# Optimization experiments

Hardware: AMD Instinct MI355X
Metric: run time of the kernel (lower is better)

Reference implementation:

```python
import jax, jax.numpy as jnp
import numpy as np

N_NODES = 100000
N_EDGES = 1600000
C_IN = 64
C_OUT = 64
BN_EPS = 1e-5


def setup_inputs() -> dict:
    key = jax.random.key(0)
    k_x, k_e, k_w, k_b, k_g = jax.random.split(key, 5)
    x = jax.random.normal(k_x, (N_NODES, C_IN), dtype=jnp.float32)
    edge_index = jax.random.randint(k_e, (2, N_EDGES), 0, N_NODES, dtype=jnp.int64)
    # Linear(in_channels*2, out_channels)
    lim = 1.0 / np.sqrt(2 * C_IN)
    W = jax.random.uniform(k_w, (2 * C_IN, C_OUT), dtype=jnp.float32, minval=-lim, maxval=lim)
    b = jax.random.uniform(k_b, (C_OUT,), dtype=jnp.float32, minval=-lim, maxval=lim)
    # BatchNorm affine params
    gamma = jnp.ones((C_OUT,), dtype=jnp.float32)
    beta = jnp.zeros((C_OUT,), dtype=jnp.float32)
    return {"x": x, "edge_index": edge_index, "W": W, "b": b, "gamma": gamma, "beta": beta}


def reference(x, edge_index, W, b, gamma, beta):
    src = edge_index[0]  # j (source)
    dst = edge_index[1]  # i (target)
    x_i = x[dst]                      # [E, C_IN]
    x_j = x[src]                      # [E, C_IN]
    # EdgeConv message: mlp(concat(x_i, x_j - x_i))
    feat = jnp.concatenate([x_i, x_j - x_i], axis=-1)  # [E, 2*C_IN]
    msg = feat @ W + b                                  # [E, C_OUT]
    # max aggregation back to target nodes; empty nodes -> 0 (PyG convention)
    agg = jax.ops.segment_max(msg, dst, num_segments=N_NODES)
    agg = jnp.where(jnp.isneginf(agg), 0.0, agg)
    h = jax.nn.elu(agg)
    # BatchNorm1d over nodes (training-mode batch stats, biased variance)
    mean = jnp.mean(h, axis=0)
    var = jnp.var(h, axis=0)
    return gamma * (h - mean) / jnp.sqrt(var + BN_EPS) + beta
```

## Files before the change

### kernel.cpp

```cpp
#include <hip/hip_runtime.h>
#include <math.h>

#define N_NODES 100000
#define N_EDGES 1600000
#define C 64
#define BKT_SHIFT 6
#define BKT_NODES 64
#define NBKT 1563
#define BKT_CAP 2048
#define TILE 8192
#define NBINB 196
#define NGEMB 391
#define MAXW 65
#define NSTRIPE 32
#define XSTR 72
#define BN_EPS 1e-5f

typedef __attribute__((ext_vector_type(8))) short short8;
typedef __attribute__((ext_vector_type(4))) float f32x4;


__device__ __forceinline__ float eluf(float x) {
    return x > 0.f ? x : (expf(x) - 1.f);
}
__device__ __forceinline__ float key32_to_f(unsigned k32) {
    unsigned k16 = k32 >> 16;
    unsigned u16 = (k16 & 0x8000u) ? (k16 & 0x7FFFu) : (~k16 & 0xFFFFu);
    return __uint_as_float(u16 << 16);
}
__device__ __forceinline__ unsigned bf16rne(float f) {
    unsigned u = __float_as_uint(f);
    return (u + 0x7FFFu + ((u >> 16) & 1u)) >> 16;
}
__device__ __forceinline__ float bf16lo_f(unsigned w) { return __uint_as_float((w & 0xFFFFu) << 16); }
__device__ __forceinline__ float bf16hi_f(unsigned w) { return __uint_as_float(w & 0xFFFF0000u); }

__device__ __forceinline__ short8 pack8(float4 a, float4 b) {
    short8 r;
    r[0] = (short)bf16rne(a.x); r[1] = (short)bf16rne(a.y);
    r[2] = (short)bf16rne(a.z); r[3] = (short)bf16rne(a.w);
    r[4] = (short)bf16rne(b.x); r[5] = (short)bf16rne(b.y);
    r[6] = (short)bf16rne(b.z); r[7] = (short)bf16rne(b.w);
    return r;
}

__global__ __launch_bounds__(256) void k_init(unsigned* __restrict__ bcnt,
                                              float* __restrict__ stripes) {
    int t = blockIdx.x * blockDim.x + threadIdx.x;
    if (t < NBKT) bcnt[t] = 0u;
    if (t < NSTRIPE * 128) stripes[t] = 0.f;
}

__global__ __launch_bounds__(1024) void k_prep(const int* __restrict__ ei,
                                               const float* __restrict__ x,
                                               const float* __restrict__ W,
                                               const float* __restrict__ b,
                                               unsigned* __restrict__ bcnt,
                                               unsigned* __restrict__ binned,
                                               unsigned* __restrict__ Apb,
                                               unsigned* __restrict__ Bkey) {
    __shared__ __align__(16) unsigned char smem[18688];
    int t = threadIdx.x;

    if (blockIdx.x < NBINB) {
        unsigned* hcnt = (unsigned*)smem;
        unsigned* hbase = hcnt + NBKT;
        int e0 = blockIdx.x * TILE;
        int ecount = min(TILE, N_EDGES - e0);

        for (int i = t; i < NBKT; i += 1024) hcnt[i] = 0u;
        __syncthreads();
        for (int i = t; i < ecount; i += 1024) {
            int dst = ei[N_EDGES + e0 + i];
            if ((unsigned)dst < N_NODES) atomicAdd(&hcnt[dst >> BKT_SHIFT], 1u);
        }
        __syncthreads();
        for (int i = t; i < NBKT; i += 1024) {
            unsigned c = hcnt[i];
            hbase[i] = c ? atomicAdd(&bcnt[i], c) : 0u;
            hcnt[i] = 0u;
        }
        __syncthreads();
        for (int i = t; i < ecount; i += 1024) {
            int src = ei[e0 + i];
            int dst = ei[N_EDGES + e0 + i];
            if ((unsigned)src >= N_NODES || (unsigned)dst >= N_NODES) continue;
            int bk = dst >> BKT_SHIFT;
            unsigned pos = hbase[bk] + atomicAdd(&hcnt[bk], 1u);
            if (pos < BKT_CAP)
                binned[(size_t)bk * BKT_CAP + pos] =
                    ((unsigned)(dst & (BKT_NODES - 1)) << 17) | (unsigned)src;
        }
    } else {
        unsigned short* WaT = (unsigned short*)smem;
        unsigned short* WbT = WaT + 64 * XSTR;
        float* biasS = (float*)(WbT + 64 * XSTR);
        int gb = blockIdx.x - NBINB;
        int base = gb * 256;

        for (int p = t; p < 4096; p += 1024) {
            int k = p >> 6, c = p & 63;
            float w1 = W[p];
            float w2 = W[4096 + p];
            WaT[c * XSTR + k] = (unsigned short)bf16rne(w1 - w2);
            WbT[c * XSTR + k] = (unsigned short)bf16rne(w2);
        }
        if (t < 64) biasS[t] = b[t];
        __syncthreads();

        int w = t >> 6;
        int l = t & 63;
        int ln = l & 15;
        int hi = l >> 4;

        short8 wa[4][2], wb[4][2];
#pragma unroll
        for (int nt = 0; nt < 4; ++nt)
#pragma unroll
            for (int h = 0; h < 2; ++h) {
                wa[nt][h] = *(const short8*)&WaT[(nt * 16 + ln) * XSTR + h * 32 + hi * 8];
                wb[nt][h] = *(const short8*)&WbT[(nt * 16 + ln) * XSTR + h * 32 + hi * 8];
            }

        int arow = base + w * 16 + ln;
        short8 af[2];
        if (arow < N_NODES) {
            const float4* xr = (const float4*)(x + (size_t)arow * 64);
#pragma unroll
            for (int h = 0; h < 2; ++h)
                af[h] = pack8(xr[h * 8 + hi * 2], xr[h * 8 + hi * 2 + 1]);
        } else {
#pragma unroll
            for (int h = 0; h < 2; ++h)
                af[h] = (short8){0, 0, 0, 0, 0, 0, 0, 0};
        }

        f32x4 acca[4], accb[4];
#pragma unroll
        for (int nt = 0; nt < 4; ++nt) {
            acca[nt] = (f32x4){0.f, 0.f, 0.f, 0.f};
            accb[nt] = (f32x4){0.f, 0.f, 0.f, 0.f};
#pragma unroll
            for (int h = 0; h < 2; ++h) {
                acca[nt] = __builtin_amdgcn_mfma_f32_16x16x32_bf16(af[h], wa[nt][h], acca[nt], 0, 0, 0);
                accb[nt] = __builtin_amdgcn_mfma_f32_16x16x32_bf16(af[h], wb[nt][h], accb[nt], 0, 0, 0);
            }
        }
#pragma unroll
        for (int nt = 0; nt < 4; ++nt) {
            int col = nt * 16 + ln;
            float bias = biasS[col];
            int cp = nt * 8 + (ln >> 1);
#pragma unroll
            for (int r = 0; r < 4; ++r) {
                int node = base + w * 16 + hi * 4 + r;
                unsigned a16 = bf16rne(acca[nt][r] + bias);
                unsigned aO = (unsigned)__shfl_xor((int)a16, 1, 64);
                unsigned r16 = bf16rne(accb[nt][r]);
                unsigned key16 = (r16 & 0x8000u) ? (~r16 & 0xFFFFu) : (r16 | 0x8000u);
                unsigned kO = (unsigned)__shfl_xor((int)key16, 1, 64);
                if (((l & 1) == 0) && node < N_NODES) {
                    Apb[(size_t)node * 32 + cp] = a16 | (aO << 16);
                    Bkey[(size_t)node * 32 + cp] = key16 | (kO << 16);
                }
            }
        }
    }
}

__global__ __launch_bounds__(256) void k_fused(const unsigned* __restrict__ bcnt,
                                               const unsigned* __restrict__ binned,
                                               const unsigned* __restrict__ Bkey,
                                               const unsigned* __restrict__ Apb,
                                               unsigned* __restrict__ hpk,
                                               float* __restrict__ stripes) {
    __shared__ __align__(16) unsigned mx[BKT_NODES * MAXW];
    int q = blockIdx.x;
    int t = threadIdx.x;
    int n0 = q * BKT_NODES;
    int nspan = min(BKT_NODES, N_NODES - n0);

    for (int i = t; i < BKT_NODES * MAXW; i += 256) mx[i] = 0u;
    __syncthreads();

    unsigned cnt = min(bcnt[q], (unsigned)BKT_CAP);
    const unsigned* lst = binned + (size_t)q * BKT_CAP;
    int ls = t & 3;
    for (unsigned i = (unsigned)(t >> 2); i < cnt; i += 64) {
        unsigned p = lst[i];
        unsigned src = p & 0x1FFFFu;
        unsigned dl = p >> 17;
        const uint4* bk = (const uint4*)(Bkey + (size_t)src * 32);
        uint4 w0 = bk[ls];
        uint4 w1 = bk[4 + ls];
        unsigned* row = mx + dl * MAXW;
        int s0 = ls * 8;
        atomicMax(&row[s0 + 0], w0.x << 16);
        atomicMax(&row[s0 + 1], w0.x & 0xFFFF0000u);
        atomicMax(&row[s0 + 2], w0.y << 16);
        atomicMax(&row[s0 + 3], w0.y & 0xFFFF0000u);
        atomicMax(&row[s0 + 4], w0.z << 16);
        atomicMax(&row[s0 + 5], w0.z & 0xFFFF0000u);
        atomicMax(&row[s0 + 6], w0.w << 16);
        atomicMax(&row[s0 + 7], w0.w & 0xFFFF0000u);
        int s1 = 32 + ls * 8;
        atomicMax(&row[s1 + 0], w1.x << 16);
        atomicMax(&row[s1 + 1], w1.x & 0xFFFF0000u);
        atomicMax(&row[s1 + 2], w1.y << 16);
        atomicMax(&row[s1 + 3], w1.y & 0xFFFF0000u);
        atomicMax(&row[s1 + 4], w1.z << 16);
        atomicMax(&row[s1 + 5], w1.z & 0xFFFF0000u);
        atomicMax(&row[s1 + 6], w1.w << 16);
        atomicMax(&row[s1 + 7], w1.w & 0xFFFF0000u);
    }
    __syncthreads();

    int lane4 = t & 15;
    int g = t >> 4;
    float4 s = make_float4(0.f, 0.f, 0.f, 0.f);
    float4 sq = make_float4(0.f, 0.f, 0.f, 0.f);
    for (int nl = g; nl < nspan; nl += 16) {
        int n = n0 + nl;
        const unsigned* row = mx + nl * MAXW + lane4 * 4;
        unsigned k0 = row[0], k1 = row[1], k2 = row[2], k3 = row[3];
        uint2 ap = *reinterpret_cast<const uint2*>(Apb + (size_t)n * 32 + lane4 * 2);
        float h0 = (k0 == 0u) ? 0.f : eluf(bf16lo_f(ap.x) + key32_to_f(k0));
        float h1 = (k1 == 0u) ? 0.f : eluf(bf16hi_f(ap.x) + key32_to_f(k1));
        float h2 = (k2 == 0u) ? 0.f : eluf(bf16lo_f(ap.y) + key32_to_f(k2));
        float h3 = (k3 == 0u) ? 0.f : eluf(bf16hi_f(ap.y) + key32_to_f(k3));
        unsigned q0 = bf16rne(h0), q1 = bf16rne(h1), q2 = bf16rne(h2), q3 = bf16rne(h3);
        uint2 hp;
        hp.x = q0 | (q1 << 16);
        hp.y = q2 | (q3 << 16);
        *reinterpret_cast<uint2*>(hpk + (size_t)n * 32 + lane4 * 2) = hp;
        float f0 = __uint_as_float(q0 << 16), f1 = __uint_as_float(q1 << 16);
        float f2 = __uint_as_float(q2 << 16), f3 = __uint_as_float(q3 << 16);
        s.x += f0; s.y += f1; s.z += f2; s.w += f3;
        sq.x += f0 * f0; sq.y += f1 * f1; sq.z += f2 * f2; sq.w += f3 * f3;
    }
    __syncthreads();

    float4* lsum = (float4*)mx;
    float4* lqum = lsum + 256;
    lsum[t] = s;
    lqum[t] = sq;
    __syncthreads();
#pragma unroll
    for (int off = 8; off >= 1; off >>= 1) {
        if (g < off) {
            int o = t + off * 16;
            lsum[t].x += lsum[o].x; lsum[t].y += lsum[o].y; lsum[t].z += lsum[o].z; lsum[t].w += lsum[o].w;
            lqum[t].x += lqum[o].x; lqum[t].y += lqum[o].y; lqum[t].z += lqum[o].z; lqum[t].w += lqum[o].w;
        }
        __syncthreads();
    }
    if (g == 0) {
        float* sb = stripes + (q & (NSTRIPE - 1)) * 128;
        int c4 = lane4 * 4;
        atomicAdd(&sb[c4 + 0], lsum[t].x);
        atomicAdd(&sb[c4 + 1], lsum[t].y);
        atomicAdd(&sb[c4 + 2], lsum[t].z);
        atomicAdd(&sb[c4 + 3], lsum[t].w);
        atomicAdd(&sb[64 + c4 + 0], lqum[t].x);
        atomicAdd(&sb[64 + c4 + 1], lqum[t].y);
        atomicAdd(&sb[64 + c4 + 2], lqum[t].z);
        atomicAdd(&sb[64 + c4 + 3], lqum[t].w);
    }
}

__global__ __launch_bounds__(128) void k_reduce(const float* __restrict__ stripes,
                                                float* __restrict__ finals) {
    int t = threadIdx.x;
    float acc = 0.f;
#pragma unroll
    for (int s = 0; s < NSTRIPE; ++s) acc += stripes[s * 128 + t];
    finals[t] = acc;
}

__global__ __launch_bounds__(256) void k_bn(const uint2* __restrict__ hpk2,
                                            const float* __restrict__ finals,
                                            const float* __restrict__ gamma,
                                            const float* __restrict__ beta,
                                            float4* __restrict__ out4) {
    size_t i = (size_t)blockIdx.x * blockDim.x + threadIdx.x;
    size_t stride = (size_t)gridDim.x * blockDim.x;
    const float invN = 1.f / (float)N_NODES;
    size_t total4 = (size_t)N_NODES * C / 4;
    for (size_t p = i; p < total4; p += stride) {
        int c4 = (int)(p & 15) * 4;
        uint2 hp = hpk2[p];
        float hx = bf16lo_f(hp.x), hy = bf16hi_f(hp.x);
        float hz = bf16lo_f(hp.y), hw = bf16hi_f(hp.y);
        float4 o;
        float m, v, inv;
        m = finals[c4 + 0] * invN; v = finals[64 + c4 + 0] * invN - m * m; inv = rsqrtf(v + BN_EPS);
        o.x = gamma[c4 + 0] * (hx - m) * inv + beta[c4 + 0];
        m = finals[c4 + 1] * invN; v = finals[64 + c4 + 1] * invN - m * m; inv = rsqrtf(v + BN_EPS);
        o.y = gamma[c4 + 1] * (hy - m) * inv + beta[c4 + 1];
        m = finals[c4 + 2] * invN; v = finals[64 + c4 + 2] * invN - m * m; inv = rsqrtf(v + BN_EPS);
        o.z = gamma[c4 + 2] * (hz - m) * inv + beta[c4 + 2];
        m = finals[c4 + 3] * invN; v = finals[64 + c4 + 3] * invN - m * m; inv = rsqrtf(v + BN_EPS);
        o.w = gamma[c4 + 3] * (hw - m) * inv + beta[c4 + 3];
        out4[p] = o;
    }
}

extern "C" void kernel_launch(void* const* d_in, const int* in_sizes, int n_in,
                              void* d_out, int out_size, void* d_ws, size_t ws_size,
                              hipStream_t stream) {
    const float* x = (const float*)d_in[0];
    const int* ei = (const int*)d_in[1];
    const float* W = (const float*)d_in[2];
    const float* b = (const float*)d_in[3];
    const float* gamma = (const float*)d_in[4];
    const float* beta = (const float*)d_in[5];
    float* out = (float*)d_out;

    char* ws = (char*)d_ws;
    unsigned* Bkey = (unsigned*)ws;
    unsigned* binned = (unsigned*)(ws + (size_t)N_NODES * 32 * 4);
    unsigned* Apb = (unsigned*)((char*)binned + (size_t)NBKT * BKT_CAP * 4);
    unsigned* hpk = Apb + (size_t)N_NODES * 32;
    unsigned* bcnt = hpk + (size_t)N_NODES * 32;
    float* stripes = (float*)((char*)bcnt + ((NBKT * 4 + 255) & ~255));
    float* finals = stripes + NSTRIPE * 128;

    k_init<<<(NSTRIPE * 128 + NBKT + 255) / 256, 256, 0, stream>>>(bcnt, stripes);
    k_prep<<<NBINB + NGEMB, 1024, 0, stream>>>(ei, x, W, b, bcnt, binned, Apb, Bkey);
    k_fused<<<NBKT, 256, 0, stream>>>(bcnt, binned, Bkey, Apb, hpk, stripes);
    k_reduce<<<1, 128, 0, stream>>>(stripes, finals);
    k_bn<<<2048, 256, 0, stream>>>((const uint2*)hpk, finals, gamma, beta, (float4*)out);
}
```

Before: 86.11 us.

## Replace global-atomic bucket binning with per-tile prefix tables and XCD-aware block remap

A new histogram kernel computes, for each edge tile, a per-bucket exclusive prefix table. The binning pass then writes edges into tile-local contiguous ranges without global atomics or a fixed bucket capacity. The aggregation kernel rebuilds each bucket's edge list by prefix-summing the 196 tile ranges and binary-searching per edge. Blocks are also remapped so that consecutive buckets land on the same XCD. This removes global atomic contention and overflow truncation, at the cost of an extra pass over the edge indices, scans in shared memory, and scattered reads of the binned data.

New measurement: 84.99 us. Within noise of the previous version (-1.3%).

```diff
diff --git a/kernel.cpp b/kernel.cpp
--- a/kernel.cpp
+++ b/kernel.cpp
@@ -7,10 +7,10 @@
 #define BKT_SHIFT 6
 #define BKT_NODES 64
 #define NBKT 1563
-#define BKT_CAP 2048
 #define TILE 8192
 #define NBINB 196
 #define NGEMB 391
+#define PSTR 1564
 #define MAXW 65
 #define NSTRIPE 32
 #define XSTR 72
@@ -44,18 +44,51 @@
     return r;
 }
 
-__global__ __launch_bounds__(256) void k_init(unsigned* __restrict__ bcnt,
-                                              float* __restrict__ stripes) {
-    int t = blockIdx.x * blockDim.x + threadIdx.x;
-    if (t < NBKT) bcnt[t] = 0u;
-    if (t < NSTRIPE * 128) stripes[t] = 0.f;
+__global__ __launch_bounds__(1024) void k_hist(const int* __restrict__ ei,
+                                               unsigned* __restrict__ tab,
+                                               float* __restrict__ stripes) {
+    __shared__ unsigned hc[NBKT];
+    __shared__ unsigned ss[1024];
+    int t = threadIdx.x;
+    int tile = blockIdx.x;
+    int e0 = tile * TILE;
+    int ecount = min(TILE, N_EDGES - e0);
+
+    for (int i = t; i < NBKT; i += 1024) hc[i] = 0u;
+    if (blockIdx.x == 0) {
+        for (int i = t; i < NSTRIPE * 128; i += 1024) stripes[i] = 0.f;
+    }
+    __syncthreads();
+    for (int i = t; i < ecount; i += 1024) {
+        int src = ei[e0 + i];
+        int dst = ei[N_EDGES + e0 + i];
+        if ((unsigned)src < N_NODES && (unsigned)dst < N_NODES)
+            atomicAdd(&hc[dst >> BKT_SHIFT], 1u);
+    }
+    __syncthreads();
+    unsigned v0 = (2 * t < NBKT) ? hc[2 * t] : 0u;
+    unsigned v1 = (2 * t + 1 < NBKT) ? hc[2 * t + 1] : 0u;
+    unsigned s = v0 + v1;
+    ss[t] = s;
+    __syncthreads();
+    for (int off = 1; off < 1024; off <<= 1) {
+        unsigned v = (t >= off) ? ss[t - off] : 0u;
+        __syncthreads();
+        ss[t] += v;
+        __syncthreads();
+    }
+    unsigned excl = ss[t] - s;
+    unsigned* row = tab + (size_t)tile * PSTR;
+    if (2 * t < NBKT) row[2 * t] = excl;
+    if (2 * t + 1 < NBKT) row[2 * t + 1] = excl + v0;
+    if (t == 1023) row[NBKT] = ss[1023];
 }
 
 __global__ __launch_bounds__(1024) void k_prep(const int* __restrict__ ei,
                                                const float* __restrict__ x,
                                                const float* __restrict__ W,
                                                const float* __restrict__ b,
-                                               unsigned* __restrict__ bcnt,
+                                               const unsigned* __restrict__ tab,
                                                unsigned* __restrict__ binned,
                                                unsigned* __restrict__ Apb,
                                                unsigned* __restrict__ Bkey) {
@@ -63,33 +96,21 @@
     int t = threadIdx.x;
 
     if (blockIdx.x < NBINB) {
-        unsigned* hcnt = (unsigned*)smem;
-        unsigned* hbase = hcnt + NBKT;
-        int e0 = blockIdx.x * TILE;
+        unsigned* cur = (unsigned*)smem;
+        int tile = blockIdx.x;
+        int e0 = tile * TILE;
         int ecount = min(TILE, N_EDGES - e0);
-
-        for (int i = t; i < NBKT; i += 1024) hcnt[i] = 0u;
-        __syncthreads();
-        for (int i = t; i < ecount; i += 1024) {
-            int dst = ei[N_EDGES + e0 + i];
-            if ((unsigned)dst < N_NODES) atomicAdd(&hcnt[dst >> BKT_SHIFT], 1u);
-        }
-        __syncthreads();
-        for (int i = t; i < NBKT; i += 1024) {
-            unsigned c = hcnt[i];
-            hbase[i] = c ? atomicAdd(&bcnt[i], c) : 0u;
-            hcnt[i] = 0u;
-        }
+        const unsigned* row = tab + (size_t)tile * PSTR;
+        for (int i = t; i < NBKT; i += 1024) cur[i] = row[i];
         __syncthreads();
         for (int i = t; i < ecount; i += 1024) {
             int src = ei[e0 + i];
             int dst = ei[N_EDGES + e0 + i];
             if ((unsigned)src >= N_NODES || (unsigned)dst >= N_NODES) continue;
             int bk = dst >> BKT_SHIFT;
-            unsigned pos = hbase[bk] + atomicAdd(&hcnt[bk], 1u);
-            if (pos < BKT_CAP)
-                binned[(size_t)bk * BKT_CAP + pos] =
-                    ((unsigned)(dst & (BKT_NODES - 1)) << 17) | (unsigned)src;
+            unsigned pos = atomicAdd(&cur[bk], 1u);
+            binned[(size_t)tile * TILE + pos] =
+                ((unsigned)(dst & (BKT_NODES - 1)) << 17) | (unsigned)src;
         }
     } else {
         unsigned short* WaT = (unsigned short*)smem;
@@ -168,26 +189,56 @@
     }
 }
 
-__global__ __launch_bounds__(256) void k_fused(const unsigned* __restrict__ bcnt,
+__global__ __launch_bounds__(256) void k_fused(const unsigned* __restrict__ tab,
                                                const unsigned* __restrict__ binned,
                                                const unsigned* __restrict__ Bkey,
                                                const unsigned* __restrict__ Apb,
                                                unsigned* __restrict__ hpk,
                                                float* __restrict__ stripes) {
     __shared__ __align__(16) unsigned mx[BKT_NODES * MAXW];
-    int q = blockIdx.x;
+    __shared__ unsigned rstart[NBINB];
+    __shared__ unsigned rb[257];
     int t = threadIdx.x;
+    int orig = blockIdx.x;
+    int xcd = orig & 7;
+    int j = orig >> 3;
+    int q = (xcd < 3 ? xcd * 196 : 3 * 196 + (xcd - 3) * 195) + j;
     int n0 = q * BKT_NODES;
     int nspan = min(BKT_NODES, N_NODES - n0);
 
     for (int i = t; i < BKT_NODES * MAXW; i += 256) mx[i] = 0u;
-    __syncthreads();
-
-    unsigned cnt = min(bcnt[q], (unsigned)BKT_CAP);
-    const unsigned* lst = binned + (size_t)q * BKT_CAP;
+
+    unsigned own = 0;
+    if (t < NBINB) {
+        unsigned rs = tab[(size_t)t * PSTR + q];
+        unsigned re = tab[(size_t)t * PSTR + q + 1];
+        rstart[t] = rs;
+        own = re - rs;
+    }
+    rb[t] = own;
+    __syncthreads();
+    for (int off = 1; off < 256; off <<= 1) {
+        unsigned v = (t >= off) ? rb[t - off] : 0u;
+        __syncthreads();
+        rb[t] += v;
+        __syncthreads();
+    }
+    unsigned excl = rb[t] - own;
+    __syncthreads();
+    rb[t] = excl;
+    if (t == 255) rb[256] = excl + own;
+    __syncthreads();
+    unsigned cnt = rb[256];
+
     int ls = t & 3;
-    for (unsigned i = (unsigned)(t >> 2); i < cnt; i += 64) {
-        unsigned p = lst[i];
+    for (unsigned idx = (unsigned)(t >> 2); idx < cnt; idx += 64) {
+        unsigned lo = 0, hi = NBINB;
+#pragma unroll
+        for (int it = 0; it < 8; ++it) {
+            unsigned mid = (lo + hi) >> 1;
+            if (rb[mid] <= idx) lo = mid; else hi = mid;
+        }
+        unsigned p = binned[(size_t)lo * TILE + rstart[lo] + (idx - rb[lo])];
         unsigned src = p & 0x1FFFFu;
         unsigned dl = p >> 17;
         const uint4* bk = (const uint4*)(Bkey + (size_t)src * 32);
@@ -318,16 +369,16 @@
 
     char* ws = (char*)d_ws;
     unsigned* Bkey = (unsigned*)ws;
-    unsigned* binned = (unsigned*)(ws + (size_t)N_NODES * 32 * 4);
-    unsigned* Apb = (unsigned*)((char*)binned + (size_t)NBKT * BKT_CAP * 4);
+    unsigned* binned = Bkey + (size_t)N_NODES * 32;
+    unsigned* Apb = binned + (size_t)NBINB * TILE;
     unsigned* hpk = Apb + (size_t)N_NODES * 32;
-    unsigned* bcnt = hpk + (size_t)N_NODES * 32;
-    float* stripes = (float*)((char*)bcnt + ((NBKT * 4 + 255) & ~255));
+    unsigned* tab = hpk + (size_t)N_NODES * 32;
+    float* stripes = (float*)(tab + (size_t)NBINB * PSTR);
     float* finals = stripes + NSTRIPE * 128;
 
-    k_init<<<(NSTRIPE * 128 + NBKT + 255) / 256, 256, 0, stream>>>(bcnt, stripes);
-    k_prep<<<NBINB + NGEMB, 1024, 0, stream>>>(ei, x, W, b, bcnt, binned, Apb, Bkey);
-    k_fused<<<NBKT, 256, 0, stream>>>(bcnt, binned, Bkey, Apb, hpk, stripes);
+    k_hist<<<NBINB, 1024, 0, stream>>>(ei, tab, stripes);
+    k_prep<<<NBINB + NGEMB, 1024, 0, stream>>>(ei, x, W, b, tab, binned, Apb, Bkey);
+    k_fused<<<NBKT, 256, 0, stream>>>(tab, binned, Bkey, Apb, hpk, stripes);
     k_reduce<<<1, 128, 0, stream>>>(stripes, finals);
     k_bn<<<2048, 256, 0, stream>>>((const uint2*)hpk, finals, gamma, beta, (float4*)out);
 }
```
